# Performance work log

Hardware: AMD Instinct MI355X
Metric: run time of the kernel (lower is better)

Reference implementation:

```python
import jax, jax.numpy as jnp
import numpy as np

W = 5      # window size
H = 4      # num heads (num_channels)
EPS = 1e-6

def rmsnorm(x, w):
    return x * w * jax.lax.rsqrt(jnp.mean(x * x, axis=-1, keepdims=True) + EPS)

def dwconv3d(x, k):
    # x: [B,D0,D1,D2,C], k: [3,3,3,1,C] depthwise 3x3x3 conv, SAME padding
    return jax.lax.conv_general_dilated(
        x, k, (1, 1, 1), 'SAME',
        dimension_numbers=('NDHWC', 'DHWIO', 'NDHWC'),
        feature_group_count=x.shape[-1])

def _part(t):
    # [B,D0,D1,D2,C] -> [B*nw, W^3, C] non-overlapping 3D windows
    B, D0, D1, D2, C = t.shape
    t = t.reshape(B, D0 // W, W, D1 // W, W, D2 // W, W, C)
    t = t.transpose(0, 1, 3, 5, 2, 4, 6, 7)
    return t.reshape(-1, W ** 3, C)

def _unpart(t, B, D0, D1, D2):
    C = t.shape[-1]
    t = t.reshape(B, D0 // W, D1 // W, D2 // W, W, W, W, C)
    t = t.transpose(0, 1, 4, 2, 5, 3, 6, 7)
    return t.reshape(B, D0, D1, D2, C)

def _pool01(t):
    # mean-pool poolable_dims=(0,1) by factor W -> coarse grid
    B, D0, D1, D2, C = t.shape
    return t.reshape(B, D0 // W, W, D1 // W, W, D2, C).mean(axis=(2, 4))

def _mha(q, k, v):
    # q,k,v: [N, L, C] -> [N, L, C] multi-head attention
    N, L, C = q.shape
    dh = C // H
    q = q.reshape(N, L, H, dh)
    k = k.reshape(N, L, H, dh)
    v = v.reshape(N, L, H, dh)
    s = jnp.einsum('nqhd,nkhd->nhqk', q, k) * (1.0 / np.sqrt(dh))
    p = jax.nn.softmax(s, axis=-1)
    return jnp.einsum('nhqk,nkhd->nqhd', p, v).reshape(N, L, C)

def _hier_attn(x, qkv_w, qkv_b, proj_w, proj_b, dw_pre, dw_post, lr_down, lr_up):
    B, D0, D1, D2, C = x.shape
    # conv_position='both': pre depthwise-conv positional term
    xin = x + dwconv3d(x, dw_pre)
    qkv = xin @ qkv_w + qkv_b                     # [B,D0,D1,D2,3C]
    q, k, v = jnp.split(qkv, 3, axis=-1)
    # fine scale: windowed local attention in W^3 blocks
    fine = _unpart(_mha(_part(q), _part(k), _part(v)), B, D0, D1, D2)
    # coarse scale: pool dims (0,1) by W, global attention over coarse tokens
    qc, kc, vc = _pool01(q), _pool01(k), _pool01(v)
    Nc = qc.shape[1] * qc.shape[2] * qc.shape[3]
    oc = _mha(qc.reshape(B, Nc, C), kc.reshape(B, Nc, C), vc.reshape(B, Nc, C))
    oc = oc.reshape(B, D0 // W, D1 // W, D2, C)
    oc = jnp.repeat(jnp.repeat(oc, W, axis=1), W, axis=2)   # upsample to full grid
    # lowrank hierarchical merge of coarse branch into fine branch
    merged = fine + (oc @ lr_down) @ lr_up
    out = merged @ proj_w + proj_b
    out = out + xin                               # attn_residual
    out = out + dwconv3d(out, dw_post)            # post conv position
    return out

def setup_inputs() -> dict:
    key = jax.random.key(0)
    ks = jax.random.split(key, 8)
    B, D0, D1, D2, C = 4, 40, 40, 20, 256
    rank = C // 4
    s = 0.02
    return {
        'x': jax.random.normal(ks[0], (B, D0, D1, D2, C), jnp.float32),
        'norm1_w': jnp.ones((C,), jnp.float32),
        'attn_norm_w': jnp.ones((C,), jnp.float32),
        'qkv_w': jax.random.normal(ks[1], (C, 3 * C), jnp.float32) * s,
        'qkv_b': jnp.zeros((3 * C,), jnp.float32),
        'proj_w': jax.random.normal(ks[2], (C, C), jnp.float32) * s,
        'proj_b': jnp.zeros((C,), jnp.float32),
        'dw_pre': jax.random.normal(ks[3], (3, 3, 3, 1, C), jnp.float32) * s,
        'dw_post': jax.random.normal(ks[4], (3, 3, 3, 1, C), jnp.float32) * s,
        'lr_down': jax.random.normal(ks[5], (C, rank), jnp.float32) * s,
        'lr_up': jax.random.normal(ks[6], (rank, C), jnp.float32) * s,
    }

def reference(x, norm1_w, attn_norm_w, qkv_w, qkv_b, proj_w, proj_b,
              dw_pre, dw_post, lr_down, lr_up) -> jnp.ndarray:
    # x = x + attn_norm(hier_attn(norm1(x)))   (dropout inactive in eval)
    a = _hier_attn(rmsnorm(x, norm1_w), qkv_w, qkv_b, proj_w, proj_b,
                   dw_pre, dw_post, lr_down, lr_up)
    return x + rmsnorm(a, attn_norm_w)
```

## Files before the change

kernel.cpp:

```cpp
#include <hip/hip_runtime.h>

#define D0c 40
#define D1c 40
#define D2c 20
#define NVOX 128000

typedef __attribute__((ext_vector_type(4))) float f4;
typedef __attribute__((ext_vector_type(8))) __bf16 bf8;
typedef __attribute__((ext_vector_type(8))) unsigned short u8s;

static __device__ __forceinline__ unsigned short f2bf(float f) {
  union { float f; unsigned int u; } v; v.f = f;
  unsigned int r = v.u + 0x7fffu + ((v.u >> 16) & 1u);
  return (unsigned short)(r >> 16);
}
static __device__ __forceinline__ float bf2f(unsigned short h) {
  union { unsigned int u; float f; } v; v.u = ((unsigned int)h) << 16;
  return v.f;
}

#define MFMA16(a, b, c) __builtin_amdgcn_mfma_f32_16x16x32_bf16((a), (b), (c), 0, 0, 0)

static __device__ __forceinline__ void gload16(const void* g, void* l) {
  __builtin_amdgcn_global_load_lds((const __attribute__((address_space(1))) unsigned int*)g,
                                   (__attribute__((address_space(3))) unsigned int*)l, 16, 0, 0);
}

__global__ __launch_bounds__(256) void k_prepw(const float* __restrict__ qkv_w,
                                               const float* __restrict__ proj_w,
                                               unsigned short* __restrict__ wq,
                                               unsigned short* __restrict__ wp) {
  int id = blockIdx.x * 256 + threadIdx.x;
  if (id < 768 * 256) {
    int kk = id & 31, row = (id >> 5) & 127, kc = (id >> 12) & 7, nt = id >> 15;
    int s = kk >> 3, kj = kk & 7;
    int g = s ^ ((row >> 1) & 3);
    int k = kc * 32 + g * 8 + kj;
    int n = nt * 128 + row;
    wq[id] = f2bf(qkv_w[k * 768 + n]);
  } else {
    int j = id - 768 * 256;
    int m = j >> 8, k = j & 255;
    wp[j] = f2bf(proj_w[k * 256 + m]);
  }
}

__global__ __launch_bounds__(256) void k_rms1(const float* __restrict__ x,
                                              const float* __restrict__ w,
                                              unsigned short* __restrict__ xn) {
  int wv = threadIdx.x >> 6, ln = threadIdx.x & 63;
  int n = blockIdx.x * 4 + wv;
  f4 v = ((const f4*)(x + (size_t)n * 256))[ln];
  float ss = v.x * v.x + v.y * v.y + v.z * v.z + v.w * v.w;
#pragma unroll
  for (int m = 32; m >= 1; m >>= 1) ss += __shfl_xor(ss, m);
  float rs = rsqrtf(ss * (1.f / 256.f) + 1e-6f);
  f4 wv4 = ((const f4*)w)[ln];
  ushort4 o;
  o.x = f2bf(v.x * wv4.x * rs); o.y = f2bf(v.y * wv4.y * rs);
  o.z = f2bf(v.z * wv4.z * rs); o.w = f2bf(v.w * wv4.w * rs);
  ((ushort4*)(xn + (size_t)n * 256))[ln] = o;
}

__global__ __launch_bounds__(256) void k_convpre(const unsigned short* __restrict__ xn,
                                                 const float* __restrict__ dw,
                                                 unsigned short* __restrict__ xin) {
  __shared__ float wl[6912];
  for (int i = threadIdx.x; i < 6912; i += 256) wl[i] = dw[i];
  __syncthreads();
  int wv = threadIdx.x >> 6, ln = threadIdx.x & 63;
  int col = blockIdx.x * 4 + wv;
  int z1 = col % D1c; int t = col / D1c; int z0 = t % D0c; int b = t / D0c;
  int c0 = ln * 4;

  const unsigned short* base[9];
  bool val[9];
#pragma unroll
  for (int c = 0; c < 9; c++) {
    int dy = c / 3 - 1, dx = c % 3 - 1;
    int y0 = z0 + dy, y1 = z1 + dx;
    val[c] = ((unsigned)y0 < (unsigned)D0c) && ((unsigned)y1 < (unsigned)D1c);
    int yy0 = val[c] ? y0 : z0, yy1 = val[c] ? y1 : z1;
    base[c] = xn + ((size_t)((b * D0c + yy0) * D1c + yy1) * D2c) * 256 + c0;
  }
  f4 a0 = {0.f,0.f,0.f,0.f}, a1 = {0.f,0.f,0.f,0.f}, a2 = {0.f,0.f,0.f,0.f};
  ushort4 nxt[9];
#pragma unroll
  for (int c = 0; c < 9; c++) {
    ushort4 ld = {0, 0, 0, 0};
    if (val[c]) ld = *(const ushort4*)(base[c]);
    nxt[c] = ld;
  }
  unsigned short* op = xin + ((size_t)col * D2c) * 256 + c0;

  for (int z = 0; z < 20; z++) {
    f4 cf[9];
#pragma unroll
    for (int c = 0; c < 9; c++) {
      cf[c].x = bf2f(nxt[c].x); cf[c].y = bf2f(nxt[c].y);
      cf[c].z = bf2f(nxt[c].z); cf[c].w = bf2f(nxt[c].w);
    }
    int zn = (z < 19) ? (z + 1) : 19;
#pragma unroll
    for (int c = 0; c < 9; c++) {
      ushort4 ld = {0, 0, 0, 0};
      if (val[c]) ld = *(const ushort4*)(base[c] + (size_t)zn * 256);
      nxt[c] = ld;
    }
#pragma unroll
    for (int c = 0; c < 9; c++) {
      const f4 w0 = *(const f4*)&wl[(c * 3 + 0) * 256 + c0];
      const f4 w1 = *(const f4*)&wl[(c * 3 + 1) * 256 + c0];
      const f4 w2 = *(const f4*)&wl[(c * 3 + 2) * 256 + c0];
      a0.x += w2.x * cf[c].x; a0.y += w2.y * cf[c].y; a0.z += w2.z * cf[c].z; a0.w += w2.w * cf[c].w;
      a1.x += w1.x * cf[c].x; a1.y += w1.y * cf[c].y; a1.z += w1.z * cf[c].z; a1.w += w1.w * cf[c].w;
      a2.x += w0.x * cf[c].x; a2.y += w0.y * cf[c].y; a2.z += w0.z * cf[c].z; a2.w += w0.w * cf[c].w;
    }
    a1.x += cf[4].x; a1.y += cf[4].y; a1.z += cf[4].z; a1.w += cf[4].w;
    if (z >= 1) {
      ushort4 o;
      o.x = f2bf(a0.x); o.y = f2bf(a0.y); o.z = f2bf(a0.z); o.w = f2bf(a0.w);
      *(ushort4*)op = o;
      op += 256;
    }
    a0 = a1; a1 = a2; a2 = (f4){0.f,0.f,0.f,0.f};
  }
  {
    ushort4 o;
    o.x = f2bf(a0.x); o.y = f2bf(a0.y); o.z = f2bf(a0.z); o.w = f2bf(a0.w);
    *(ushort4*)op = o;
  }
}

__global__ __launch_bounds__(256) void k_gemm_qkv(const unsigned short* __restrict__ a_bf,
                                                  const unsigned short* __restrict__ wq2,
                                                  const float* __restrict__ bias,
                                                  unsigned short* __restrict__ out) {
  __shared__ unsigned short As[16384];
  __shared__ unsigned short Bs[8192];
  int m0 = blockIdx.x * 64;
  int tid = threadIdx.x;
  int w = tid >> 6, l = tid & 63;
  int wr = w >> 1, wc = w & 1;
  int lrow = l & 15, lg = l >> 4;

  {
    const char* Ab = (const char*)(a_bf + (size_t)m0 * 256);
    int row = tid >> 2, s = tid & 3;
    int g = s ^ ((row >> 1) & 3);
    const char* src0 = Ab + row * 512 + g * 16;
    char* dst0 = ((char*)As) + w * 1024 + l * 16;
#pragma unroll
    for (int kc = 0; kc < 8; kc++)
      gload16(src0 + kc * 64, dst0 + kc * 4096);
  }
  {
    const char* gB = (const char*)wq2;
    char* lB = (char*)Bs;
    gload16(gB + tid * 16, lB + w * 1024 + l * 16);
    gload16(gB + 4096 + tid * 16, lB + 4096 + w * 1024 + l * 16);
  }

  int buf = 0;
  f4 acc[2][4];
  for (int nt = 0; nt < 6; nt++) {
    float bvv[4];
#pragma unroll
    for (int j = 0; j < 4; j++) bvv[j] = bias[nt * 128 + wc * 64 + j * 16 + lrow];
#pragma unroll
    for (int i = 0; i < 2; i++)
#pragma unroll
      for (int j = 0; j < 4; j++) acc[i][j] = {0.f, 0.f, 0.f, 0.f};

    for (int kc = 0; kc < 8; kc++) {
      int t = nt * 8 + kc;
      if (t + 1 < 48) {
        const char* gB = (const char*)wq2 + (size_t)(t + 1) * 8192;
        char* lB = ((char*)Bs) + (buf ^ 1) * 8192;
        gload16(gB + tid * 16, lB + w * 1024 + l * 16);
        gload16(gB + 4096 + tid * 16, lB + 4096 + w * 1024 + l * 16);
        asm volatile("s_waitcnt vmcnt(2)\n\ts_barrier" ::: "memory");
      } else {
        asm volatile("s_waitcnt vmcnt(0)\n\ts_barrier" ::: "memory");
      }
      bf8 af[2], bf_[4];
#pragma unroll
      for (int i = 0; i < 2; i++) {
        int row = wr * 32 + i * 16 + lrow;
        af[i] = *(const bf8*)&As[kc * 2048 + row * 32 + ((lg ^ ((row >> 1) & 3)) * 8)];
      }
#pragma unroll
      for (int j = 0; j < 4; j++) {
        int rowb = wc * 64 + j * 16 + lrow;
        bf_[j] = *(const bf8*)&Bs[buf * 4096 + rowb * 32 + ((lg ^ ((rowb >> 1) & 3)) * 8)];
      }
#pragma unroll
      for (int i = 0; i < 2; i++)
#pragma unroll
        for (int j = 0; j < 4; j++) acc[i][j] = MFMA16(af[i], bf_[j], acc[i][j]);
      asm volatile("s_barrier" ::: "memory");
      buf ^= 1;
    }

    unsigned short* Cs = &Bs[(buf ^ 1) * 4096];
    int crow = tid >> 3, cseg = tid & 7;
#pragma unroll
    for (int h = 0; h < 2; h++) {
      if (wr == h) {
#pragma unroll
        for (int i = 0; i < 2; i++)
#pragma unroll
          for (int j = 0; j < 4; j++)
#pragma unroll
            for (int r = 0; r < 4; r++)
              Cs[(i * 16 + lg * 4 + r) * 128 + wc * 64 + j * 16 + lrow] =
                  f2bf(acc[i][j][r] + bvv[j]);
      }
      asm volatile("s_waitcnt lgkmcnt(0)\n\ts_barrier" ::: "memory");
      {
        u8s v0 = *(const u8s*)&Cs[crow * 128 + cseg * 16];
        u8s v1 = *(const u8s*)&Cs[crow * 128 + cseg * 16 + 8];
        unsigned short* orow = out + (size_t)(m0 + h * 32 + crow) * 768 + nt * 128 + cseg * 16;
        *(u8s*)orow = v0;
        *(u8s*)(orow + 8) = v1;
      }
      asm volatile("s_waitcnt lgkmcnt(0)\n\ts_barrier" ::: "memory");
    }
  }
}

__global__ __launch_bounds__(256) void k_fineattn(const unsigned short* __restrict__ qkv,
                                                  unsigned short* __restrict__ fine) {
  __shared__ unsigned short sm[27136];
  unsigned short* Qs = sm;
  unsigned short* Ks = sm + 9216;
  unsigned short* Vt = sm + 18432;
  unsigned short* Ps = sm;
  int h = blockIdx.x & 3, wid = blockIdx.x >> 2;
  int w2 = wid & 3, w1 = (wid >> 2) & 7, w0 = (wid >> 5) & 7, b = wid >> 8;
  int tid = threadIdx.x;
  int tok = tid >> 1, half = tid & 1;
  if (tok < 125) {
    int i0 = tok / 25, rr = tok % 25, i1 = rr / 5, i2 = rr % 5;
    int n = ((b * D0c + w0 * 5 + i0) * D1c + w1 * 5 + i1) * D2c + w2 * 5 + i2;
    const u8s* qp = (const u8s*)(qkv + (size_t)n * 768 + h * 64 + half * 32);
    const u8s* kp = (const u8s*)(qkv + (size_t)n * 768 + 256 + h * 64 + half * 32);
    const unsigned short* vp = qkv + (size_t)n * 768 + 512 + h * 64 + half * 32;
#pragma unroll
    for (int e = 0; e < 4; e++) {
      *(u8s*)&Qs[tok * 72 + half * 32 + e * 8] = qp[e];
      *(u8s*)&Ks[tok * 72 + half * 32 + e * 8] = kp[e];
    }
#pragma unroll
    for (int d = 0; d < 32; d++) Vt[(half * 32 + d) * 136 + tok] = vp[d];
  } else {
    u8s z = {0, 0, 0, 0, 0, 0, 0, 0};
#pragma unroll
    for (int e = 0; e < 4; e++) {
      *(u8s*)&Qs[tok * 72 + half * 32 + e * 8] = z;
      *(u8s*)&Ks[tok * 72 + half * 32 + e * 8] = z;
    }
#pragma unroll
    for (int d = 0; d < 32; d++) Vt[(half * 32 + d) * 136 + tok] = 0;
  }
  __syncthreads();
  int wv = tid >> 6, ln = tid & 63, lrow = ln & 15, lg = ln >> 4;
  f4 s[2][8];
#pragma unroll
  for (int mi = 0; mi < 2; mi++)
#pragma unroll
    for (int ni = 0; ni < 8; ni++) s[mi][ni] = {0.f, 0.f, 0.f, 0.f};
  bf8 aq[2][2];
#pragma unroll
  for (int ks = 0; ks < 2; ks++)
#pragma unroll
    for (int mi = 0; mi < 2; mi++)
      aq[mi][ks] = *(const bf8*)&Qs[(wv * 32 + mi * 16 + lrow) * 72 + ks * 32 + lg * 8];
#pragma unroll
  for (int ni = 0; ni < 8; ni++) {
#pragma unroll
    for (int ks = 0; ks < 2; ks++) {
      bf8 bk = *(const bf8*)&Ks[(ni * 16 + lrow) * 72 + ks * 32 + lg * 8];
      s[0][ni] = MFMA16(aq[0][ks], bk, s[0][ni]);
      s[1][ni] = MFMA16(aq[1][ks], bk, s[1][ni]);
    }
  }
#pragma unroll
  for (int mi = 0; mi < 2; mi++) {
#pragma unroll
    for (int j = 0; j < 4; j++) {
      float mx = -3e38f;
#pragma unroll
      for (int ni = 0; ni < 8; ni++) {
        int col = ni * 16 + lrow;
        float v = (col < 125) ? s[mi][ni][j] * 0.125f : -3e38f;
        s[mi][ni][j] = v;
        mx = fmaxf(mx, v);
      }
#pragma unroll
      for (int m = 8; m >= 1; m >>= 1) mx = fmaxf(mx, __shfl_xor(mx, m));
      float sum = 0.f;
#pragma unroll
      for (int ni = 0; ni < 8; ni++) {
        float p = __expf(s[mi][ni][j] - mx);
        s[mi][ni][j] = p;
        sum += p;
      }
#pragma unroll
      for (int m = 8; m >= 1; m >>= 1) sum += __shfl_xor(sum, m);
      float inv = 1.f / sum;
#pragma unroll
      for (int ni = 0; ni < 8; ni++) s[mi][ni][j] *= inv;
    }
  }
  __syncthreads();
#pragma unroll
  for (int mi = 0; mi < 2; mi++)
#pragma unroll
    for (int ni = 0; ni < 8; ni++)
#pragma unroll
      for (int j = 0; j < 4; j++)
        Ps[(wv * 32 + mi * 16 + lg * 4 + j) * 136 + ni * 16 + lrow] = f2bf(s[mi][ni][j]);
  __syncthreads();
  f4 o[2][4];
#pragma unroll
  for (int mi = 0; mi < 2; mi++)
#pragma unroll
    for (int ni = 0; ni < 4; ni++) o[mi][ni] = {0.f, 0.f, 0.f, 0.f};
#pragma unroll
  for (int ks = 0; ks < 4; ks++) {
    bf8 ap0 = *(const bf8*)&Ps[(wv * 32 + 0 + lrow) * 136 + ks * 32 + lg * 8];
    bf8 ap1 = *(const bf8*)&Ps[(wv * 32 + 16 + lrow) * 136 + ks * 32 + lg * 8];
#pragma unroll
    for (int ni = 0; ni < 4; ni++) {
      bf8 bv = *(const bf8*)&Vt[(ni * 16 + lrow) * 136 + ks * 32 + lg * 8];
      o[0][ni] = MFMA16(ap0, bv, o[0][ni]);
      o[1][ni] = MFMA16(ap1, bv, o[1][ni]);
    }
  }
#pragma unroll
  for (int mi = 0; mi < 2; mi++) {
    int rt0 = wv * 32 + mi * 16 + lg * 4;
#pragma unroll
    for (int r = 0; r < 4; r++) {
      int tk = rt0 + r;
      if (tk >= 125) continue;
      int i0 = tk / 25, rr = tk % 25, i1 = rr / 5, i2 = rr % 5;
      int n = ((b * D0c + w0 * 5 + i0) * D1c + w1 * 5 + i1) * D2c + w2 * 5 + i2;
#pragma unroll
      for (int ni = 0; ni < 4; ni++)
        fine[(size_t)n * 256 + h * 64 + ni * 16 + lrow] = f2bf(o[mi][ni][r]);
    }
  }
}

__global__ __launch_bounds__(256) void k_pool(const unsigned short* __restrict__ qkv,
                                              unsigned short* __restrict__ qc,
                                              unsigned short* __restrict__ kc,
                                              unsigned short* __restrict__ vct) {
  int ct = blockIdx.x;
  int z2 = ct % 20; int t = ct / 20; int c1 = t & 7; int c0 = (t >> 3) & 7; int b = t >> 6;
  int tid = threadIdx.x;
  float a0 = 0.f, a1 = 0.f, a2 = 0.f;
  for (int i0 = 0; i0 < 5; i0++)
    for (int i1 = 0; i1 < 5; i1++) {
      int n = ((b * D0c + c0 * 5 + i0) * D1c + c1 * 5 + i1) * D2c + z2;
      const unsigned short* row = qkv + (size_t)n * 768;
      a0 += bf2f(row[tid]);
      a1 += bf2f(row[tid + 256]);
      a2 += bf2f(row[tid + 512]);
    }
  const float sc = 1.f / 25.f;
  qc[(size_t)ct * 256 + tid] = f2bf(a0 * sc);
  kc[(size_t)ct * 256 + tid] = f2bf(a1 * sc);
  int h = tid >> 6, d = tid & 63;
  int tk = ct - b * 1280;
  vct[(((size_t)b * 4 + h) * 64 + d) * 1288 + tk] = f2bf(a2 * sc);
}

__global__ __launch_bounds__(256) void k_coarse(const unsigned short* __restrict__ qc,
                                                const unsigned short* __restrict__ kc,
                                                const unsigned short* __restrict__ vct,
                                                float* __restrict__ oc) {
  __shared__ unsigned short Qs[9216];
  __shared__ unsigned short KP[9216];
  __shared__ unsigned short Vts[4608];
  int qt = blockIdx.x;
  int b = blockIdx.y >> 2, h = blockIdx.y & 3;
  int tid = threadIdx.x, wv = tid >> 6, ln = tid & 63, lrow = ln & 15, lg = ln >> 4;
  {
    int tk = tid >> 1, half = tid & 1;
    const u8s* qp = (const u8s*)(qc + (size_t)(b * 1280 + qt * 128 + tk) * 256 + h * 64 + half * 32);
#pragma unroll
    for (int e = 0; e < 4; e++) *(u8s*)&Qs[tk * 72 + half * 32 + e * 8] = qp[e];
  }
  float mrun[2][4], srun[2][4];
  f4 o[2][4];
#pragma unroll
  for (int mi = 0; mi < 2; mi++)
#pragma unroll
    for (int j = 0; j < 4; j++) { mrun[mi][j] = -3e38f; srun[mi][j] = 0.f; }
#pragma unroll
  for (int mi = 0; mi < 2; mi++)
#pragma unroll
    for (int ni = 0; ni < 4; ni++) o[mi][ni] = {0.f, 0.f, 0.f, 0.f};

  int ktok = tid >> 2, kq = (tid & 3) * 16;
  int vd = tid >> 2, vtc = (tid & 3) * 16;

  for (int kt = 0; kt < 20; kt++) {
    {
      const u8s* kp = (const u8s*)(kc + (size_t)(b * 1280 + kt * 64 + ktok) * 256 + h * 64 + kq);
      *(u8s*)&KP[ktok * 72 + kq] = kp[0];
      *(u8s*)&KP[ktok * 72 + kq + 8] = kp[1];
      const u8s* vp = (const u8s*)(vct + (((size_t)b * 4 + h) * 64 + vd) * 1288 + kt * 64 + vtc);
      *(u8s*)&Vts[vd * 72 + vtc] = vp[0];
      *(u8s*)&Vts[vd * 72 + vtc + 8] = vp[1];
    }
    __syncthreads();
    f4 s[2][4];
#pragma unroll
    for (int mi = 0; mi < 2; mi++)
#pragma unroll
      for (int ni = 0; ni < 4; ni++) s[mi][ni] = {0.f, 0.f, 0.f, 0.f};
    bf8 aq[2][2];
#pragma unroll
    for (int ks = 0; ks < 2; ks++)
#pragma unroll
      for (int mi = 0; mi < 2; mi++)
        aq[mi][ks] = *(const bf8*)&Qs[(wv * 32 + mi * 16 + lrow) * 72 + ks * 32 + lg * 8];
#pragma unroll
    for (int ni = 0; ni < 4; ni++) {
#pragma unroll
      for (int ks = 0; ks < 2; ks++) {
        bf8 bk = *(const bf8*)&KP[(ni * 16 + lrow) * 72 + ks * 32 + lg * 8];
        s[0][ni] = MFMA16(aq[0][ks], bk, s[0][ni]);
        s[1][ni] = MFMA16(aq[1][ks], bk, s[1][ni]);
      }
    }
#pragma unroll
    for (int mi = 0; mi < 2; mi++) {
#pragma unroll
      for (int j = 0; j < 4; j++) {
        float mx = -3e38f;
#pragma unroll
        for (int ni = 0; ni < 4; ni++) {
          float v = s[mi][ni][j] * 0.125f;
          s[mi][ni][j] = v;
          mx = fmaxf(mx, v);
        }
#pragma unroll
        for (int m = 8; m >= 1; m >>= 1) mx = fmaxf(mx, __shfl_xor(mx, m));
        float nm = fmaxf(mrun[mi][j], mx);
        float alpha = __expf(mrun[mi][j] - nm);
        mrun[mi][j] = nm;
        float sum = 0.f;
#pragma unroll
        for (int ni = 0; ni < 4; ni++) {
          float p = __expf(s[mi][ni][j] - nm);
          s[mi][ni][j] = p;
          sum += p;
        }
#pragma unroll
        for (int m = 8; m >= 1; m >>= 1) sum += __shfl_xor(sum, m);
        srun[mi][j] = srun[mi][j] * alpha + sum;
#pragma unroll
        for (int ni = 0; ni < 4; ni++) o[mi][ni][j] *= alpha;
      }
    }
    __syncthreads();
#pragma unroll
    for (int mi = 0; mi < 2; mi++)
#pragma unroll
      for (int ni = 0; ni < 4; ni++)
#pragma unroll
        for (int j = 0; j < 4; j++)
          KP[(wv * 32 + mi * 16 + lg * 4 + j) * 72 + ni * 16 + lrow] = f2bf(s[mi][ni][j]);
    __syncthreads();
#pragma unroll
    for (int ks = 0; ks < 2; ks++) {
      bf8 ap0 = *(const bf8*)&KP[(wv * 32 + 0 + lrow) * 72 + ks * 32 + lg * 8];
      bf8 ap1 = *(const bf8*)&KP[(wv * 32 + 16 + lrow) * 72 + ks * 32 + lg * 8];
#pragma unroll
      for (int ni = 0; ni < 4; ni++) {
        bf8 bv = *(const bf8*)&Vts[(ni * 16 + lrow) * 72 + ks * 32 + lg * 8];
        o[0][ni] = MFMA16(ap0, bv, o[0][ni]);
        o[1][ni] = MFMA16(ap1, bv, o[1][ni]);
      }
    }
    __syncthreads();
  }
#pragma unroll
  for (int mi = 0; mi < 2; mi++)
#pragma unroll
    for (int j = 0; j < 4; j++) {
      float inv = 1.f / srun[mi][j];
      int row = qt * 128 + wv * 32 + mi * 16 + lg * 4 + j;
      float* orow = oc + ((size_t)(b * 1280 + row)) * 256 + h * 64;
#pragma unroll
      for (int ni = 0; ni < 4; ni++) orow[ni * 16 + lrow] = o[mi][ni][j] * inv;
    }
}

__global__ __launch_bounds__(256) void k_lowrank(const float* __restrict__ oc,
                                                 const float* __restrict__ lrd,
                                                 const float* __restrict__ lru,
                                                 float* __restrict__ oclr) {
  __shared__ float tmp[16 * 64];
  int t0 = blockIdx.x * 16;
  int tid = threadIdx.x;
  int i = tid >> 4, r4 = (tid & 15) * 4;
  f4 a = {0.f, 0.f, 0.f, 0.f};
  const float* orow = oc + (size_t)(t0 + i) * 256;
  for (int k = 0; k < 256; k++) {
    float ov = orow[k];
    const f4 w = *(const f4*)&lrd[k * 64 + r4];
    a.x += ov * w.x; a.y += ov * w.y; a.z += ov * w.z; a.w += ov * w.w;
  }
  *(f4*)&tmp[i * 64 + r4] = a;
  __syncthreads();
  int c16 = (tid & 15) * 16;
  f4 acc0 = {0.f,0.f,0.f,0.f}, acc1 = {0.f,0.f,0.f,0.f}, acc2 = {0.f,0.f,0.f,0.f}, acc3 = {0.f,0.f,0.f,0.f};
  for (int r = 0; r < 64; r++) {
    float tv = tmp[i * 64 + r];
    const f4* wr = (const f4*)&lru[r * 256 + c16];
    f4 w0 = wr[0], w1 = wr[1], w2 = wr[2], w3 = wr[3];
    acc0.x += tv * w0.x; acc0.y += tv * w0.y; acc0.z += tv * w0.z; acc0.w += tv * w0.w;
    acc1.x += tv * w1.x; acc1.y += tv * w1.y; acc1.z += tv * w1.z; acc1.w += tv * w1.w;
    acc2.x += tv * w2.x; acc2.y += tv * w2.y; acc2.z += tv * w2.z; acc2.w += tv * w2.w;
    acc3.x += tv * w3.x; acc3.y += tv * w3.y; acc3.z += tv * w3.z; acc3.w += tv * w3.w;
  }
  float* outr = oclr + (size_t)(t0 + i) * 256 + c16;
  *(f4*)&outr[0] = acc0; *(f4*)&outr[4] = acc1; *(f4*)&outr[8] = acc2; *(f4*)&outr[12] = acc3;
}

__global__ __launch_bounds__(256) void k_gemm_proj(const unsigned short* __restrict__ fine,
                                                   const float* __restrict__ oclr,
                                                   const unsigned short* __restrict__ wt,
                                                   const float* __restrict__ bias,
                                                   const unsigned short* __restrict__ xin,
                                                   unsigned short* __restrict__ out1) {
  __shared__ unsigned short As[128 * 40];
  __shared__ unsigned short Bs[128 * 40];
  int m0 = blockIdx.y * 128, n0 = blockIdx.x * 128;
  int tid = threadIdx.x;
  int wv = tid >> 6, ln = tid & 63;
  int wr = wv >> 1, wc = wv & 1;
  int lrow = ln & 15, lg = ln >> 4;
  f4 acc[4][4];
#pragma unroll
  for (int i = 0; i < 4; i++)
#pragma unroll
    for (int j = 0; j < 4; j++) acc[i][j] = {0.f, 0.f, 0.f, 0.f};
  int srow = tid >> 1, sk = (tid & 1) * 16;
  int nrow = m0 + srow;
  int z2 = nrow % D2c; int tt = nrow / D2c; int z1 = tt % D1c; tt /= D1c; int z0 = tt % D0c; int bb = tt / D0c;
  int ct = ((bb * 8 + z0 / 5) * 8 + z1 / 5) * 20 + z2;
  for (int k0 = 0; k0 < 256; k0 += 32) {
    const unsigned short* fp = fine + (size_t)nrow * 256 + k0 + sk;
    const float* cp = oclr + (size_t)ct * 256 + k0 + sk;
    u8s f0 = *(const u8s*)fp, f1 = *(const u8s*)(fp + 8);
    u8s t0, t1;
#pragma unroll
    for (int e = 0; e < 8; e++) {
      t0[e] = f2bf(bf2f(f0[e]) + cp[e]);
      t1[e] = f2bf(bf2f(f1[e]) + cp[8 + e]);
    }
    *(u8s*)&As[srow * 40 + sk] = t0;
    *(u8s*)&As[srow * 40 + sk + 8] = t1;
    const u8s* bp = (const u8s*)(wt + (size_t)(n0 + srow) * 256 + k0 + sk);
    *(u8s*)&Bs[srow * 40 + sk] = bp[0];
    *(u8s*)&Bs[srow * 40 + sk + 8] = bp[1];
    __syncthreads();
    bf8 af[4], bf_[4];
#pragma unroll
    for (int i = 0; i < 4; i++) af[i] = *(const bf8*)&As[(wr * 64 + i * 16 + lrow) * 40 + lg * 8];
#pragma unroll
    for (int j = 0; j < 4; j++) bf_[j] = *(const bf8*)&Bs[(wc * 64 + j * 16 + lrow) * 40 + lg * 8];
#pragma unroll
    for (int i = 0; i < 4; i++)
#pragma unroll
      for (int j = 0; j < 4; j++) acc[i][j] = MFMA16(af[i], bf_[j], acc[i][j]);
    __syncthreads();
  }
#pragma unroll
  for (int j = 0; j < 4; j++) {
    int col = n0 + wc * 64 + j * 16 + lrow;
    float bv = bias[col];
#pragma unroll
    for (int i = 0; i < 4; i++) {
      int row = m0 + wr * 64 + i * 16 + lg * 4;
#pragma unroll
      for (int r = 0; r < 4; r++) {
        float xr = bf2f(xin[(size_t)(row + r) * 256 + col]);
        out1[(size_t)(row + r) * 256 + col] = f2bf(acc[i][j][r] + bv + xr);
      }
    }
  }
}

__global__ __launch_bounds__(256) void k_convpost(const unsigned short* __restrict__ o1,
                                                  const float* __restrict__ dw,
                                                  const float* __restrict__ x,
                                                  const float* __restrict__ anw,
                                                  float* __restrict__ outp) {
  __shared__ float wl[6912];
  for (int i = threadIdx.x; i < 6912; i += 256) wl[i] = dw[i];
  __syncthreads();
  int wv = threadIdx.x >> 6, ln = threadIdx.x & 63;
  int col = blockIdx.x * 4 + wv;
  int z1 = col % D1c; int t = col / D1c; int z0 = t % D0c; int b = t / D0c;
  int c0 = ln * 4;

  const unsigned short* base[9];
  bool val[9];
#pragma unroll
  for (int c = 0; c < 9; c++) {
    int dy = c / 3 - 1, dx = c % 3 - 1;
    int y0 = z0 + dy, y1 = z1 + dx;
    val[c] = ((unsigned)y0 < (unsigned)D0c) && ((unsigned)y1 < (unsigned)D1c);
    int yy0 = val[c] ? y0 : z0, yy1 = val[c] ? y1 : z1;
    base[c] = o1 + ((size_t)((b * D0c + yy0) * D1c + yy1) * D2c) * 256 + c0;
  }
  f4 a0 = {0.f,0.f,0.f,0.f}, a1 = {0.f,0.f,0.f,0.f}, a2 = {0.f,0.f,0.f,0.f};
  ushort4 nxt[9];
#pragma unroll
  for (int c = 0; c < 9; c++) {
    ushort4 ld = {0, 0, 0, 0};
    if (val[c]) ld = *(const ushort4*)(base[c]);
    nxt[c] = ld;
  }
  const f4 wv4 = *(const f4*)(anw + c0);
  const float* xp = x + ((size_t)col * D2c) * 256 + c0;
  float* op = outp + ((size_t)col * D2c) * 256 + c0;

  for (int z = 0; z < 20; z++) {
    f4 cf[9];
#pragma unroll
    for (int c = 0; c < 9; c++) {
      cf[c].x = bf2f(nxt[c].x); cf[c].y = bf2f(nxt[c].y);
      cf[c].z = bf2f(nxt[c].z); cf[c].w = bf2f(nxt[c].w);
    }
    int zn = (z < 19) ? (z + 1) : 19;
#pragma unroll
    for (int c = 0; c < 9; c++) {
      ushort4 ld = {0, 0, 0, 0};
      if (val[c]) ld = *(const ushort4*)(base[c] + (size_t)zn * 256);
      nxt[c] = ld;
    }
#pragma unroll
    for (int c = 0; c < 9; c++) {
      const f4 w0 = *(const f4*)&wl[(c * 3 + 0) * 256 + c0];
      const f4 w1 = *(const f4*)&wl[(c * 3 + 1) * 256 + c0];
      const f4 w2 = *(const f4*)&wl[(c * 3 + 2) * 256 + c0];
      a0.x += w2.x * cf[c].x; a0.y += w2.y * cf[c].y; a0.z += w2.z * cf[c].z; a0.w += w2.w * cf[c].w;
      a1.x += w1.x * cf[c].x; a1.y += w1.y * cf[c].y; a1.z += w1.z * cf[c].z; a1.w += w1.w * cf[c].w;
      a2.x += w0.x * cf[c].x; a2.y += w0.y * cf[c].y; a2.z += w0.z * cf[c].z; a2.w += w0.w * cf[c].w;
    }
    a1.x += cf[4].x; a1.y += cf[4].y; a1.z += cf[4].z; a1.w += cf[4].w;
    if (z >= 1) {
      float ss = a0.x * a0.x + a0.y * a0.y + a0.z * a0.z + a0.w * a0.w;
#pragma unroll
      for (int m = 32; m >= 1; m >>= 1) ss += __shfl_xor(ss, m);
      float rs = rsqrtf(ss * (1.f / 256.f) + 1e-6f);
      f4 xv = *(const f4*)xp;
      f4 res;
      res.x = xv.x + a0.x * wv4.x * rs;
      res.y = xv.y + a0.y * wv4.y * rs;
      res.z = xv.z + a0.z * wv4.z * rs;
      res.w = xv.w + a0.w * wv4.w * rs;
      *(f4*)op = res;
      xp += 256; op += 256;
    }
    a0 = a1; a1 = a2; a2 = (f4){0.f,0.f,0.f,0.f};
  }
  {
    float ss = a0.x * a0.x + a0.y * a0.y + a0.z * a0.z + a0.w * a0.w;
#pragma unroll
    for (int m = 32; m >= 1; m >>= 1) ss += __shfl_xor(ss, m);
    float rs = rsqrtf(ss * (1.f / 256.f) + 1e-6f);
    f4 xv = *(const f4*)xp;
    f4 res;
    res.x = xv.x + a0.x * wv4.x * rs;
    res.y = xv.y + a0.y * wv4.y * rs;
    res.z = xv.z + a0.z * wv4.z * rs;
    res.w = xv.w + a0.w * wv4.w * rs;
    *(f4*)op = res;
  }
}

extern "C" void kernel_launch(void* const* d_in, const int* in_sizes, int n_in,
                              void* d_out, int out_size, void* d_ws, size_t ws_size,
                              hipStream_t stream) {
  const float* x          = (const float*)d_in[0];
  const float* norm1_w    = (const float*)d_in[1];
  const float* attn_norm_w= (const float*)d_in[2];
  const float* qkv_w      = (const float*)d_in[3];
  const float* qkv_b      = (const float*)d_in[4];
  const float* proj_w     = (const float*)d_in[5];
  const float* proj_b     = (const float*)d_in[6];
  const float* dw_pre     = (const float*)d_in[7];
  const float* dw_post    = (const float*)d_in[8];
  const float* lr_down    = (const float*)d_in[9];
  const float* lr_up      = (const float*)d_in[10];
  float* outp = (float*)d_out;

  unsigned char* w = (unsigned char*)d_ws;
  size_t off = 0;
  unsigned short* xn   = (unsigned short*)(w + off); off += 65536000ULL;
  unsigned short* xin  = (unsigned short*)(w + off); off += 65536000ULL;
  unsigned short* qkv  = (unsigned short*)(w + off); off += 196608000ULL;
  unsigned short* out1 = (unsigned short*)(w + off); off += 65536000ULL;
  unsigned short* qc   = (unsigned short*)(w + off); off += 2621440ULL;
  unsigned short* kc   = (unsigned short*)(w + off); off += 2621440ULL;
  unsigned short* vct  = (unsigned short*)(w + off); off += 2637824ULL;
  float* oc            = (float*)(w + off);          off += 5242880ULL;
  float* oclr          = (float*)(w + off);          off += 5242880ULL;
  unsigned short* wq   = (unsigned short*)(w + off); off += 393216ULL;
  unsigned short* wp   = (unsigned short*)(w + off); off += 131072ULL;
  unsigned short* fine = xn;

  k_prepw<<<1024, 256, 0, stream>>>(qkv_w, proj_w, wq, wp);
  k_rms1<<<32000, 256, 0, stream>>>(x, norm1_w, xn);
  k_convpre<<<1600, 256, 0, stream>>>(xn, dw_pre, xin);
  k_gemm_qkv<<<2000, 256, 0, stream>>>(xin, wq, qkv_b, qkv);
  k_fineattn<<<4096, 256, 0, stream>>>(qkv, fine);
  k_pool<<<5120, 256, 0, stream>>>(qkv, qc, kc, vct);
  k_coarse<<<dim3(10, 16), 256, 0, stream>>>(qc, kc, vct, oc);
  k_lowrank<<<320, 256, 0, stream>>>(oc, lr_down, lr_up, oclr);
  k_gemm_proj<<<dim3(2, 1000), 256, 0, stream>>>(fine, oclr, wp, proj_b, xin, out1);
  k_convpost<<<1600, 256, 0, stream>>>(out1, dw_post, x, attn_norm_w, outp);
}
```

Measured before the change: 682.4 us.

## Restructure projection GEMM with full-K A tile, swizzled LDS, async double-buffered weights

The projection GEMM now uses 64-row blocks that load the whole K=256 A tile (fine plus upsampled coarse) once into XOR-swizzled LDS and loop over both 128-column output tiles. This avoids rebuilding the A operand twice across column blocks. Weight tiles are pre-swizzled in the prep kernel and streamed with global_load_lds double buffering. The epilogue goes through LDS so bias and residual are applied with coalesced 16-byte loads and stores. The cost is more barriers and a larger LDS footprint, which may reduce occupancy.

New measurement: 668.5 us. 1.02x faster.

```diff
diff --git a/kernel.cpp b/kernel.cpp
--- a/kernel.cpp
+++ b/kernel.cpp
@@ -40,8 +40,12 @@
     wq[id] = f2bf(qkv_w[k * 768 + n]);
   } else {
     int j = id - 768 * 256;
-    int m = j >> 8, k = j & 255;
-    wp[j] = f2bf(proj_w[k * 256 + m]);
+    int kk = j & 31, row = (j >> 5) & 127, kc = (j >> 12) & 7, nt = j >> 15;
+    int s = kk >> 3, kj = kk & 7;
+    int g = s ^ ((row >> 1) & 3);
+    int k = kc * 32 + g * 8 + kj;
+    int n = nt * 128 + row;
+    wp[j] = f2bf(proj_w[k * 256 + n]);
   }
 }
 
@@ -536,65 +540,121 @@
 
 __global__ __launch_bounds__(256) void k_gemm_proj(const unsigned short* __restrict__ fine,
                                                    const float* __restrict__ oclr,
-                                                   const unsigned short* __restrict__ wt,
+                                                   const unsigned short* __restrict__ wp2,
                                                    const float* __restrict__ bias,
                                                    const unsigned short* __restrict__ xin,
                                                    unsigned short* __restrict__ out1) {
-  __shared__ unsigned short As[128 * 40];
-  __shared__ unsigned short Bs[128 * 40];
-  int m0 = blockIdx.y * 128, n0 = blockIdx.x * 128;
+  __shared__ unsigned short As[16384];
+  __shared__ unsigned short Bs[8192];
+  int m0 = blockIdx.x * 64;
   int tid = threadIdx.x;
-  int wv = tid >> 6, ln = tid & 63;
-  int wr = wv >> 1, wc = wv & 1;
-  int lrow = ln & 15, lg = ln >> 4;
-  f4 acc[4][4];
-#pragma unroll
-  for (int i = 0; i < 4; i++)
-#pragma unroll
-    for (int j = 0; j < 4; j++) acc[i][j] = {0.f, 0.f, 0.f, 0.f};
-  int srow = tid >> 1, sk = (tid & 1) * 16;
-  int nrow = m0 + srow;
-  int z2 = nrow % D2c; int tt = nrow / D2c; int z1 = tt % D1c; tt /= D1c; int z0 = tt % D0c; int bb = tt / D0c;
-  int ct = ((bb * 8 + z0 / 5) * 8 + z1 / 5) * 20 + z2;
-  for (int k0 = 0; k0 < 256; k0 += 32) {
-    const unsigned short* fp = fine + (size_t)nrow * 256 + k0 + sk;
-    const float* cp = oclr + (size_t)ct * 256 + k0 + sk;
-    u8s f0 = *(const u8s*)fp, f1 = *(const u8s*)(fp + 8);
-    u8s t0, t1;
-#pragma unroll
-    for (int e = 0; e < 8; e++) {
-      t0[e] = f2bf(bf2f(f0[e]) + cp[e]);
-      t1[e] = f2bf(bf2f(f1[e]) + cp[8 + e]);
-    }
-    *(u8s*)&As[srow * 40 + sk] = t0;
-    *(u8s*)&As[srow * 40 + sk + 8] = t1;
-    const u8s* bp = (const u8s*)(wt + (size_t)(n0 + srow) * 256 + k0 + sk);
-    *(u8s*)&Bs[srow * 40 + sk] = bp[0];
-    *(u8s*)&Bs[srow * 40 + sk + 8] = bp[1];
-    __syncthreads();
-    bf8 af[4], bf_[4];
-#pragma unroll
-    for (int i = 0; i < 4; i++) af[i] = *(const bf8*)&As[(wr * 64 + i * 16 + lrow) * 40 + lg * 8];
-#pragma unroll
-    for (int j = 0; j < 4; j++) bf_[j] = *(const bf8*)&Bs[(wc * 64 + j * 16 + lrow) * 40 + lg * 8];
-#pragma unroll
-    for (int i = 0; i < 4; i++)
-#pragma unroll
-      for (int j = 0; j < 4; j++) acc[i][j] = MFMA16(af[i], bf_[j], acc[i][j]);
-    __syncthreads();
-  }
-#pragma unroll
-  for (int j = 0; j < 4; j++) {
-    int col = n0 + wc * 64 + j * 16 + lrow;
-    float bv = bias[col];
-#pragma unroll
-    for (int i = 0; i < 4; i++) {
-      int row = m0 + wr * 64 + i * 16 + lg * 4;
-#pragma unroll
-      for (int r = 0; r < 4; r++) {
-        float xr = bf2f(xin[(size_t)(row + r) * 256 + col]);
-        out1[(size_t)(row + r) * 256 + col] = f2bf(acc[i][j][r] + bv + xr);
-      }
+  int w = tid >> 6, l = tid & 63;
+  int wr = w >> 1, wc = w & 1;
+  int lrow = l & 15, lg = l >> 4;
+
+  {
+    const char* gB = (const char*)wp2;
+    char* lB = (char*)Bs;
+    gload16(gB + tid * 16, lB + w * 1024 + l * 16);
+    gload16(gB + 4096 + tid * 16, lB + 4096 + w * 1024 + l * 16);
+  }
+  {
+    int row = tid >> 2, s = tid & 3;
+    int g = s ^ ((row >> 1) & 3);
+    int nrow = m0 + row;
+    int z2 = nrow % D2c; int tt = nrow / D2c; int z1 = tt % D1c; tt /= D1c;
+    int z0 = tt % D0c; int bb = tt / D0c;
+    int ct = ((bb * 8 + z0 / 5) * 8 + z1 / 5) * 20 + z2;
+    const unsigned short* fp = fine + (size_t)nrow * 256 + g * 8;
+    const float* cp = oclr + (size_t)ct * 256 + g * 8;
+#pragma unroll
+    for (int kc = 0; kc < 8; kc++) {
+      u8s fv = *(const u8s*)(fp + kc * 32);
+      f4 cv0 = *(const f4*)(cp + kc * 32);
+      f4 cv1 = *(const f4*)(cp + kc * 32 + 4);
+      u8s t0;
+      t0[0] = f2bf(bf2f(fv[0]) + cv0.x); t0[1] = f2bf(bf2f(fv[1]) + cv0.y);
+      t0[2] = f2bf(bf2f(fv[2]) + cv0.z); t0[3] = f2bf(bf2f(fv[3]) + cv0.w);
+      t0[4] = f2bf(bf2f(fv[4]) + cv1.x); t0[5] = f2bf(bf2f(fv[5]) + cv1.y);
+      t0[6] = f2bf(bf2f(fv[6]) + cv1.z); t0[7] = f2bf(bf2f(fv[7]) + cv1.w);
+      *(u8s*)&As[kc * 2048 + row * 32 + s * 8] = t0;
+    }
+  }
+  asm volatile("s_waitcnt lgkmcnt(0)\n\ts_barrier" ::: "memory");
+
+  int buf = 0;
+  f4 acc[2][4];
+  for (int nt = 0; nt < 2; nt++) {
+    float bvv[4];
+#pragma unroll
+    for (int j = 0; j < 4; j++) bvv[j] = bias[nt * 128 + wc * 64 + j * 16 + lrow];
+#pragma unroll
+    for (int i = 0; i < 2; i++)
+#pragma unroll
+      for (int j = 0; j < 4; j++) acc[i][j] = {0.f, 0.f, 0.f, 0.f};
+
+    for (int kc = 0; kc < 8; kc++) {
+      int t = nt * 8 + kc;
+      if (t + 1 < 16) {
+        const char* gB = (const char*)wp2 + (size_t)(t + 1) * 8192;
+        char* lB = ((char*)Bs) + (buf ^ 1) * 8192;
+        gload16(gB + tid * 16, lB + w * 1024 + l * 16);
+        gload16(gB + 4096 + tid * 16, lB + 4096 + w * 1024 + l * 16);
+        asm volatile("s_waitcnt vmcnt(2)\n\ts_barrier" ::: "memory");
+      } else {
+        asm volatile("s_waitcnt vmcnt(0)\n\ts_barrier" ::: "memory");
+      }
+      bf8 af[2], bf_[4];
+#pragma unroll
+      for (int i = 0; i < 2; i++) {
+        int row = wr * 32 + i * 16 + lrow;
+        af[i] = *(const bf8*)&As[kc * 2048 + row * 32 + ((lg ^ ((row >> 1) & 3)) * 8)];
+      }
+#pragma unroll
+      for (int j = 0; j < 4; j++) {
+        int rowb = wc * 64 + j * 16 + lrow;
+        bf_[j] = *(const bf8*)&Bs[buf * 4096 + rowb * 32 + ((lg ^ ((rowb >> 1) & 3)) * 8)];
+      }
+#pragma unroll
+      for (int i = 0; i < 2; i++)
+#pragma unroll
+        for (int j = 0; j < 4; j++) acc[i][j] = MFMA16(af[i], bf_[j], acc[i][j]);
+      asm volatile("s_barrier" ::: "memory");
+      buf ^= 1;
+    }
+
+    unsigned short* Cs = &Bs[(buf ^ 1) * 4096];
+    int crow = tid >> 3, cseg = tid & 7;
+#pragma unroll
+    for (int h = 0; h < 2; h++) {
+      if (wr == h) {
+#pragma unroll
+        for (int i = 0; i < 2; i++)
+#pragma unroll
+          for (int j = 0; j < 4; j++)
+#pragma unroll
+            for (int r = 0; r < 4; r++)
+              Cs[(i * 16 + lg * 4 + r) * 128 + wc * 64 + j * 16 + lrow] =
+                  f2bf(acc[i][j][r] + bvv[j]);
+      }
+      asm volatile("s_waitcnt lgkmcnt(0)\n\ts_barrier" ::: "memory");
+      {
+        u8s v0 = *(const u8s*)&Cs[crow * 128 + cseg * 16];
+        u8s v1 = *(const u8s*)&Cs[crow * 128 + cseg * 16 + 8];
+        const unsigned short* xrow = xin + (size_t)(m0 + h * 32 + crow) * 256 + nt * 128 + cseg * 16;
+        u8s x0 = *(const u8s*)xrow;
+        u8s x1 = *(const u8s*)(xrow + 8);
+        u8s o0, o1;
+#pragma unroll
+        for (int e = 0; e < 8; e++) {
+          o0[e] = f2bf(bf2f(v0[e]) + bf2f(x0[e]));
+          o1[e] = f2bf(bf2f(v1[e]) + bf2f(x1[e]));
+        }
+        unsigned short* orow = out1 + (size_t)(m0 + h * 32 + crow) * 256 + nt * 128 + cseg * 16;
+        *(u8s*)orow = o0;
+        *(u8s*)(orow + 8) = o1;
+      }
+      asm volatile("s_waitcnt lgkmcnt(0)\n\ts_barrier" ::: "memory");
     }
   }
 }
@@ -728,6 +788,6 @@
   k_pool<<<5120, 256, 0, stream>>>(qkv, qc, kc, vct);
   k_coarse<<<dim3(10, 16), 256, 0, stream>>>(qc, kc, vct, oc);
   k_lowrank<<<320, 256, 0, stream>>>(oc, lr_down, lr_up, oclr);
-  k_gemm_proj<<<dim3(2, 1000), 256, 0, stream>>>(fine, oclr, wp, proj_b, xin, out1);
+  k_gemm_proj<<<2000, 256, 0, stream>>>(fine, oclr, wp, proj_b, xin, out1);
   k_convpost<<<1600, 256, 0, stream>>>(out1, dw_post, x, attn_norm_w, outp);
 }
```
